# Kernel tuning notes

Measured on AMD Instinct MI355X. Metric: run time of the kernel, lower is better.

## Reference

```python
import jax, jax.numpy as jnp
import numpy as np

K = 3
PAD = 1
KK = K * K
GROUPS = 32  # min(32, dim) with dim=64
EPS = 1e-5


def _conv(x, w, pad):
    return jax.lax.conv_general_dilated(
        x, w, (1, 1), [(pad, pad), (pad, pad)],
        dimension_numbers=('NCHW', 'OIHW', 'NCHW'))


def _bilinear_gather(x, py, px):
    # x: (B,C,H,W); py,px: (B,KK,H,W) float sampling coords (zero pad outside)
    B, C, H, W = x.shape
    xf = x.reshape(B, C, H * W)
    y0f = jnp.floor(py)
    x0f = jnp.floor(px)
    wy1 = py - y0f  # fractional weights (differentiable path to offsets)
    wx1 = px - x0f
    y0 = y0f.astype(jnp.int32)
    x0 = x0f.astype(jnp.int32)

    def g(yi, xi):
        valid = (yi >= 0) & (yi < H) & (xi >= 0) & (xi < W)
        idx = (jnp.clip(yi, 0, H - 1) * W + jnp.clip(xi, 0, W - 1)).reshape(B, 1, -1)
        v = jnp.take_along_axis(xf, idx, axis=2).reshape(B, C, KK, H, W)
        return v * valid[:, None].astype(x.dtype)

    v00 = g(y0, x0)
    v01 = g(y0, x0 + 1)
    v10 = g(y0 + 1, x0)
    v11 = g(y0 + 1, x0 + 1)
    wy1e = wy1[:, None]
    wx1e = wx1[:, None]
    return (v00 * (1 - wy1e) * (1 - wx1e) + v01 * (1 - wy1e) * wx1e
            + v10 * wy1e * (1 - wx1e) + v11 * wy1e * wx1e)


def _forward(x, w_off1, w_off2, w_mask1, w_mask2, weight, bias, gamma, beta):
    B, C, H, W = x.shape
    # offset branch: 1x1 conv then KxK conv -> (B, 2*KK, H, W)
    off = _conv(_conv(x, w_off1, 0), w_off2, PAD).reshape(B, KK, 2, H, W)
    # mask branch -> sigmoid modulation (B, KK, H, W)
    mask = jax.nn.sigmoid(_conv(_conv(x, w_mask1, 0), w_mask2, PAD))
    # base kernel grid (torchvision deform_conv2d: pairs are (dy, dx) per tap)
    ky = jnp.repeat(jnp.arange(K) - PAD, K).astype(x.dtype)
    kx = jnp.tile(jnp.arange(K) - PAD, K).astype(x.dtype)
    py = off[:, :, 0] + jnp.arange(H, dtype=x.dtype)[None, None, :, None] + ky[None, :, None, None]
    px = off[:, :, 1] + jnp.arange(W, dtype=x.dtype)[None, None, None, :] + kx[None, :, None, None]
    samp = _bilinear_gather(x, py, px)  # (B, C, KK, H, W)
    # depthwise deformable conv: per-channel weight over KK taps, modulated by mask
    out = jnp.einsum('bkhw,ck,bckhw->bchw', mask, weight.reshape(C, KK), samp)
    out = out + bias[None, :, None, None]
    # GroupNorm(32, C)
    g = out.reshape(B, GROUPS, C // GROUPS, H, W)
    mu = g.mean(axis=(2, 3, 4), keepdims=True)
    var = g.var(axis=(2, 3, 4), keepdims=True)
    gn = ((g - mu) * jax.lax.rsqrt(var + EPS)).reshape(B, C, H, W)
    gn = gn * gamma[None, :, None, None] + beta[None, :, None, None]
    return jax.nn.gelu(gn, approximate=False)


def setup_inputs() -> dict:
    key = jax.random.key(0)
    ks = jax.random.split(key, 6)
    B, C, H, W = 4, 64, 128, 128
    x = jax.random.normal(ks[0], (B, C, H, W), dtype=jnp.float32)
    w_off1 = jax.random.normal(ks[1], (C, C, 1, 1), dtype=jnp.float32) * 0.05
    w_off2 = jax.random.normal(ks[2], (2 * KK, C, K, K), dtype=jnp.float32) * 0.02
    w_mask1 = jax.random.normal(ks[3], (C, C, 1, 1), dtype=jnp.float32) * 0.05
    w_mask2 = jax.random.normal(ks[4], (KK, C, K, K), dtype=jnp.float32) * 0.05
    bound = 1.0 / np.sqrt(KK)  # kaiming_uniform(a=1) for (C,1,K,K) -> fan_in=KK
    weight = jax.random.uniform(ks[5], (C, 1, K, K), dtype=jnp.float32,
                                minval=-bound, maxval=bound)
    bias = jnp.zeros((C,), dtype=jnp.float32)
    gamma = jnp.ones((C,), dtype=jnp.float32)
    beta = jnp.zeros((C,), dtype=jnp.float32)
    return {'x': x, 'w_off1': w_off1, 'w_off2': w_off2, 'w_mask1': w_mask1,
            'w_mask2': w_mask2, 'weight': weight, 'bias': bias,
            'gamma': gamma, 'beta': beta}


def reference(x, w_off1, w_off2, w_mask1, w_mask2, weight, bias, gamma, beta):
    return _forward(x, w_off1, w_off2, w_mask1, w_mask2, weight, bias, gamma, beta)
```

## Files before the change

### kernel.cpp

```cpp
#include <hip/hip_runtime.h>
#include <math.h>

#define B_  4
#define C_  64
#define H_  128
#define W_  128
#define HW_ (H_*W_)
#define NPIX_ (B_*HW_)
#define GROUPS_ 32

typedef __attribute__((ext_vector_type(8))) short short8;
typedef __attribute__((ext_vector_type(4))) float f32x4;

__device__ inline short f2bf_rne(float f) {
    unsigned u = __float_as_uint(f);
    unsigned r = (u + 0x7FFFu + ((u >> 16) & 1u)) >> 16;
    return (short)r;
}
__device__ inline float bf2f(short h) {
    return __uint_as_float(((unsigned)(unsigned short)h) << 16);
}
__device__ inline short8 ld8(const short* p) {
    union { uint4 u; short8 s; } c;
    c.u = *(const uint4*)p;
    return c.s;
}

__global__ void k0_prep(const float* __restrict__ w_off1, const float* __restrict__ w_mask1,
                        const float* __restrict__ w_off2, const float* __restrict__ w_mask2,
                        short* __restrict__ wc_hi, short* __restrict__ wc_lo) {
    int i = blockIdx.x * 256 + threadIdx.x;
    if (i >= 32 * 576) return;
    int cout = i / 576;
    int r    = i % 576;
    int pos  = r >> 6, ci = r & 63;
    float s = 0.f;
    if (cout < 18) {
        for (int cm = 0; cm < 64; cm++)
            s += w_off2[(cout * 64 + cm) * 9 + pos] * w_off1[cm * 64 + ci];
    } else if (cout < 27) {
        for (int cm = 0; cm < 64; cm++)
            s += w_mask2[((cout - 18) * 64 + cm) * 9 + pos] * w_mask1[cm * 64 + ci];
    }
    short h = f2bf_rne(s);
    wc_hi[i] = h;
    wc_lo[i] = f2bf_rne(s - bf2f(h));
}

__global__ __launch_bounds__(256) void k1_trans(const float* __restrict__ x,
                                                short* __restrict__ xtb) {
    int l   = threadIdx.x & 63;
    int wv  = threadIdx.x >> 6;
    int row = l >> 4, col = l & 15;
    int p0  = blockIdx.x * 64 + wv * 16;
    int b   = p0 >> 14;
    int hw  = p0 & (HW_ - 1);
    const float* xb = x + (size_t)b * C_ * HW_ + hw;
#pragma unroll
    for (int kb = 0; kb < 2; kb++) {
        int ci0 = kb * 32 + row * 8;
        float xv[8];
#pragma unroll
        for (int j = 0; j < 8; j++) xv[j] = xb[(ci0 + j) * HW_ + col];
        short8 a;
#pragma unroll
        for (int j = 0; j < 8; j++) a[j] = f2bf_rne(xv[j]);
        union { short8 s; uint4 u; } cv; cv.s = a;
        *(uint4*)(xtb + ((size_t)(p0 + col)) * 64 + ci0) = cv.u;
    }
}

__global__ __launch_bounds__(256, 2) void k2_mfma(const short* __restrict__ xtb,
                                                  const short* __restrict__ wc_hi,
                                                  const short* __restrict__ wc_lo,
                                                  float* __restrict__ offmask) {
    int l   = threadIdx.x & 63;
    int wv  = threadIdx.x >> 6;
    int row = l >> 4, col = l & 15;
    int blk = blockIdx.x;
    int h   = blk & 127;
    int pb  = blk * 128 + wv * 32;
    int w0  = (pb & 127);

    const short8 zero = {0,0,0,0,0,0,0,0};
    f32x4 a00 = {0.f,0.f,0.f,0.f};
    f32x4 a01 = {0.f,0.f,0.f,0.f};
    f32x4 a10 = {0.f,0.f,0.f,0.f};
    f32x4 a11 = {0.f,0.f,0.f,0.f};

    short8 cw0, cw1, cw2, cw3, ca0, ca1;
    {
        const int pos = 0, dy = -1, dx = -1;
        int ci0 = row * 8;
        int ko  = pos * 64 + ci0;
        cw0 = ld8(wc_hi + (size_t)col * 576 + ko);
        cw1 = ld8(wc_lo + (size_t)col * 576 + ko);
        cw2 = ld8(wc_hi + (size_t)(col + 16) * 576 + ko);
        cw3 = ld8(wc_lo + (size_t)(col + 16) * 576 + ko);
#pragma unroll
        for (int mt = 0; mt < 2; mt++) {
            int pbase = pb + mt * 16 + col;
            int w = w0 + mt * 16 + col;
            bool valid = ((unsigned)(h + dy) < 128u) && ((unsigned)(w + dx) < 128u);
            int addr = valid ? (pbase + dy * 128 + dx) : pbase;
            short8 v = ld8(xtb + (size_t)addr * 64 + ci0);
            if (mt == 0) ca0 = valid ? v : zero; else ca1 = valid ? v : zero;
        }
    }

#pragma unroll
    for (int kb = 0; kb < 18; kb++) {
        short8 nw0, nw1, nw2, nw3, na0, na1;
        if (kb < 17) {
            const int kn = kb + 1;
            const int pos = kn >> 1;
            const int dy = pos / 3 - 1, dx = pos % 3 - 1;
            int ci0 = (kn & 1) * 32 + row * 8;
            int ko  = pos * 64 + ci0;
            nw0 = ld8(wc_hi + (size_t)col * 576 + ko);
            nw1 = ld8(wc_lo + (size_t)col * 576 + ko);
            nw2 = ld8(wc_hi + (size_t)(col + 16) * 576 + ko);
            nw3 = ld8(wc_lo + (size_t)(col + 16) * 576 + ko);
#pragma unroll
            for (int mt = 0; mt < 2; mt++) {
                int pbase = pb + mt * 16 + col;
                int w = w0 + mt * 16 + col;
                bool valid = ((unsigned)(h + dy) < 128u) && ((unsigned)(w + dx) < 128u);
                int addr = valid ? (pbase + dy * 128 + dx) : pbase;
                short8 v = ld8(xtb + (size_t)addr * 64 + ci0);
                if (mt == 0) na0 = valid ? v : zero; else na1 = valid ? v : zero;
            }
        }
        a00 = __builtin_amdgcn_mfma_f32_16x16x32_bf16(ca0, cw0, a00, 0, 0, 0);
        a00 = __builtin_amdgcn_mfma_f32_16x16x32_bf16(ca0, cw1, a00, 0, 0, 0);
        a01 = __builtin_amdgcn_mfma_f32_16x16x32_bf16(ca0, cw2, a01, 0, 0, 0);
        a01 = __builtin_amdgcn_mfma_f32_16x16x32_bf16(ca0, cw3, a01, 0, 0, 0);
        a10 = __builtin_amdgcn_mfma_f32_16x16x32_bf16(ca1, cw0, a10, 0, 0, 0);
        a10 = __builtin_amdgcn_mfma_f32_16x16x32_bf16(ca1, cw1, a10, 0, 0, 0);
        a11 = __builtin_amdgcn_mfma_f32_16x16x32_bf16(ca1, cw2, a11, 0, 0, 0);
        a11 = __builtin_amdgcn_mfma_f32_16x16x32_bf16(ca1, cw3, a11, 0, 0, 0);
        cw0 = nw0; cw1 = nw1; cw2 = nw2; cw3 = nw3;
        ca0 = na0; ca1 = na1;
    }

#pragma unroll
    for (int mt = 0; mt < 2; mt++) {
        f32x4 n0 = mt ? a10 : a00;
        f32x4 n1 = mt ? a11 : a01;
#pragma unroll
        for (int r = 0; r < 4; r++) {
            int p = pb + mt * 16 + row * 4 + r;
            float* om = offmask + (size_t)p * 32;
            om[col] = n0[r];
            if (col < 2)       om[16 + col] = n1[r];
            else if (col < 11) om[16 + col] = 1.f / (1.f + expf(-n1[r]));
        }
    }
}

__global__ __launch_bounds__(256) void k3_deform(const short* __restrict__ xtb,
                                                 const float* __restrict__ offmask,
                                                 const float* __restrict__ weight,
                                                 const float* __restrict__ bias,
                                                 unsigned short* __restrict__ out_pre,
                                                 float* __restrict__ partials) {
    __shared__ float wl[C_ * 9];
    __shared__ float bl[C_];
    __shared__ float lds_s[4][4][8];
    __shared__ float lds_ss[4][4][8];
    for (int i = threadIdx.x; i < C_ * 9; i += 256) wl[i] = weight[i];
    if (threadIdx.x < C_) bl[threadIdx.x] = bias[threadIdx.x];
    __syncthreads();

    int blk   = blockIdx.x;
    int xcd   = blk & 7;
    int slot  = blk >> 3;
    int b     = slot >> 5;
    int r     = (slot & 31) >> 1;
    int hrow  = slot & 1;
    int h     = xcd * 16 + r;
    int pl    = threadIdx.x >> 2;
    int chunk = threadIdx.x & 3;
    int c0    = chunk * 16;
    int w     = hrow * 64 + pl;
    int hw    = h * W_ + w;
    int P     = b * HW_ + hw;
    int slot_img = xcd * 32 + (slot & 31);

    float acc[16];
#pragma unroll
    for (int i = 0; i < 16; i++) acc[i] = 0.f;

    const float* po = offmask + (size_t)P * 32;
    const short* xb = xtb + (size_t)b * HW_ * 64;

    for (int k = 0; k < 9; k++) {
        float offy = po[2 * k];
        float offx = po[2 * k + 1];
        float mk   = po[18 + k];
        float py = offy + (float)h + (float)(k / 3 - 1);
        float px = offx + (float)w + (float)(k % 3 - 1);
        float y0f = floorf(py), x0f = floorf(px);
        int y0 = (int)y0f, x0 = (int)x0f;
        int y1 = y0 + 1,   x1 = x0 + 1;
        float wy1 = py - y0f, wx1 = px - x0f;
        float wy0 = 1.f - wy1, wx0 = 1.f - wx1;
        bool vy0 = ((unsigned)y0 < (unsigned)H_);
        bool vy1 = ((unsigned)y1 < (unsigned)H_);
        bool vx0 = ((unsigned)x0 < (unsigned)W_);
        bool vx1 = ((unsigned)x1 < (unsigned)W_);
        int cy0 = min(max(y0, 0), H_ - 1);
        int cy1 = min(max(y1, 0), H_ - 1);
        int cx0 = min(max(x0, 0), W_ - 1);
        int cx1 = min(max(x1, 0), W_ - 1);
        float b00 = wy0 * wx0 * ((vy0 && vx0) ? mk : 0.f);
        float b01 = wy0 * wx1 * ((vy0 && vx1) ? mk : 0.f);
        float b10 = wy1 * wx0 * ((vy1 && vx0) ? mk : 0.f);
        float b11 = wy1 * wx1 * ((vy1 && vx1) ? mk : 0.f);

        const short* p00 = xb + ((size_t)cy0 * W_ + cx0) * 64 + c0;
        const short* p01 = xb + ((size_t)cy0 * W_ + cx1) * 64 + c0;
        const short* p10 = xb + ((size_t)cy1 * W_ + cx0) * 64 + c0;
        const short* p11 = xb + ((size_t)cy1 * W_ + cx1) * 64 + c0;

#pragma unroll
        for (int half = 0; half < 2; half++) {
            uint4 u00 = *(const uint4*)(p00 + 8 * half);
            uint4 u01 = *(const uint4*)(p01 + 8 * half);
            uint4 u10 = *(const uint4*)(p10 + 8 * half);
            uint4 u11 = *(const uint4*)(p11 + 8 * half);
            unsigned a00[4] = {u00.x, u00.y, u00.z, u00.w};
            unsigned a01[4] = {u01.x, u01.y, u01.z, u01.w};
            unsigned a10[4] = {u10.x, u10.y, u10.z, u10.w};
            unsigned a11[4] = {u11.x, u11.y, u11.z, u11.w};
#pragma unroll
            for (int d = 0; d < 4; d++) {
                float s_lo = b00 * __uint_as_float(a00[d] << 16)
                           + b01 * __uint_as_float(a01[d] << 16)
                           + b10 * __uint_as_float(a10[d] << 16)
                           + b11 * __uint_as_float(a11[d] << 16);
                float s_hi = b00 * __uint_as_float(a00[d] & 0xFFFF0000u)
                           + b01 * __uint_as_float(a01[d] & 0xFFFF0000u)
                           + b10 * __uint_as_float(a10[d] & 0xFFFF0000u)
                           + b11 * __uint_as_float(a11[d] & 0xFFFF0000u);
                int c = 8 * half + 2 * d;
                acc[c]     += wl[(c0 + c) * 9 + k] * s_lo;
                acc[c + 1] += wl[(c0 + c + 1) * 9 + k] * s_hi;
            }
        }
    }

    unsigned short* op = out_pre + ((size_t)b * C_ + c0) * HW_ + hw;
#pragma unroll
    for (int c = 0; c < 16; c++) {
        acc[c] += bl[c0 + c];
        op[c * HW_] = (unsigned short)f2bf_rne(acc[c]);
    }

    float s8[8], ss8[8];
#pragma unroll
    for (int j = 0; j < 8; j++) {
        float a0 = acc[2 * j], a1 = acc[2 * j + 1];
        s8[j]  = a0 + a1;
        ss8[j] = a0 * a0 + a1 * a1;
    }
#pragma unroll
    for (int m = 4; m < 64; m <<= 1) {
#pragma unroll
        for (int j = 0; j < 8; j++) {
            s8[j]  += __shfl_xor(s8[j], m);
            ss8[j] += __shfl_xor(ss8[j], m);
        }
    }
    int lane = threadIdx.x & 63, wid = threadIdx.x >> 6;
    if (lane < 4) {
#pragma unroll
        for (int j = 0; j < 8; j++) {
            lds_s[wid][lane][j]  = s8[j];
            lds_ss[wid][lane][j] = ss8[j];
        }
    }
    __syncthreads();
    if (threadIdx.x < 32) {
        int g = threadIdx.x;
        int ch = g >> 3, j = g & 7;
        float S  = lds_s[0][ch][j] + lds_s[1][ch][j] + lds_s[2][ch][j] + lds_s[3][ch][j];
        float SS = lds_ss[0][ch][j] + lds_ss[1][ch][j] + lds_ss[2][ch][j] + lds_ss[3][ch][j];
        float2 v = make_float2(S, SS);
        *(float2*)(partials + (((size_t)(b * GROUPS_ + g)) * 256 + slot_img) * 2) = v;
    }
}

__global__ __launch_bounds__(256) void k4_reduce(const float* __restrict__ partials,
                                                 float* __restrict__ stats) {
    int bg = blockIdx.x;
    float2 v = ((const float2*)partials)[bg * 256 + threadIdx.x];
    float s = v.x, ss = v.y;
#pragma unroll
    for (int m = 1; m < 64; m <<= 1) {
        s  += __shfl_xor(s, m);
        ss += __shfl_xor(ss, m);
    }
    __shared__ float ls[8];
    int lane = threadIdx.x & 63, wid = threadIdx.x >> 6;
    if (lane == 0) { ls[wid] = s; ls[4 + wid] = ss; }
    __syncthreads();
    if (threadIdx.x == 0) {
        float S  = ls[0] + ls[1] + ls[2] + ls[3];
        float SS = ls[4] + ls[5] + ls[6] + ls[7];
        const float inv = 1.f / (2.f * HW_);
        float mean = S * inv;
        float var  = SS * inv - mean * mean;
        stats[bg * 2]     = mean;
        stats[bg * 2 + 1] = rsqrtf(var + 1e-5f);
    }
}

__global__ __launch_bounds__(256) void k5_norm_gelu(const unsigned short* __restrict__ out_pre,
                                                    const float* __restrict__ stats,
                                                    const float* __restrict__ gamma,
                                                    const float* __restrict__ beta,
                                                    float* __restrict__ out) {
    int i = blockIdx.x * 256 + threadIdx.x;
    int e = i << 3;
    int c = (e >> 14) & (C_ - 1);
    int b = e >> 20;
    int bg = b * GROUPS_ + (c >> 1);
    float mean = stats[bg * 2];
    float rstd = stats[bg * 2 + 1];
    float ga = gamma[c] * rstd;
    float be = beta[c] - mean * ga;
    uint4 v = ((const uint4*)out_pre)[i];
    unsigned dw[4] = {v.x, v.y, v.z, v.w};
    float4 r0, r1;
    float o[8];
#pragma unroll
    for (int d = 0; d < 4; d++) {
        float lo = __uint_as_float(dw[d] << 16);
        float hi = __uint_as_float(dw[d] & 0xFFFF0000u);
        float t0 = lo * ga + be;
        float t1 = hi * ga + be;
        o[2 * d]     = 0.5f * t0 * (1.f + erff(t0 * 0.70710678118654752f));
        o[2 * d + 1] = 0.5f * t1 * (1.f + erff(t1 * 0.70710678118654752f));
    }
    r0 = make_float4(o[0], o[1], o[2], o[3]);
    r1 = make_float4(o[4], o[5], o[6], o[7]);
    ((float4*)out)[2 * i]     = r0;
    ((float4*)out)[2 * i + 1] = r1;
}

extern "C" void kernel_launch(void* const* d_in, const int* in_sizes, int n_in,
                              void* d_out, int out_size, void* d_ws, size_t ws_size,
                              hipStream_t stream) {
    const float* x       = (const float*)d_in[0];
    const float* w_off1  = (const float*)d_in[1];
    const float* w_off2  = (const float*)d_in[2];
    const float* w_mask1 = (const float*)d_in[3];
    const float* w_mask2 = (const float*)d_in[4];
    const float* weight  = (const float*)d_in[5];
    const float* bias    = (const float*)d_in[6];
    const float* gamma   = (const float*)d_in[7];
    const float* beta    = (const float*)d_in[8];
    float* out = (float*)d_out;

    char* ws = (char*)d_ws;
    size_t o = 0;
    short* wc_hi = (short*)(ws + o); o += 32 * 576 * 2;
    short* wc_lo = (short*)(ws + o); o += 32 * 576 * 2;
    o = (o + 255) & ~(size_t)255;
    short* xtb               = (short*)(ws + o);          o += (size_t)NPIX_ * 64 * 2;
    float* offmask           = (float*)(ws + o);          o += (size_t)NPIX_ * 32 * 4;
    unsigned short* out_pre  = (unsigned short*)(ws + o); o += (size_t)NPIX_ * 64 * 2;
    float* partials          = (float*)(ws + o);          o += (size_t)128 * 256 * 2 * 4;
    float* stats             = (float*)(ws + o);          o += 256 * 4;

    hipLaunchKernelGGL(k0_prep, dim3(72), dim3(256), 0, stream,
                       w_off1, w_mask1, w_off2, w_mask2, wc_hi, wc_lo);
    hipLaunchKernelGGL(k1_trans, dim3(NPIX_ / 64), dim3(256), 0, stream,
                       x, xtb);
    hipLaunchKernelGGL(k2_mfma, dim3(NPIX_ / 128), dim3(256), 0, stream,
                       xtb, wc_hi, wc_lo, offmask);
    hipLaunchKernelGGL(k3_deform, dim3(NPIX_ / 64), dim3(256), 0, stream,
                       xtb, offmask, weight, bias, out_pre, partials);
    hipLaunchKernelGGL(k4_reduce, dim3(B_ * GROUPS_), dim3(256), 0, stream,
                       partials, stats);
    hipLaunchKernelGGL(k5_norm_gelu, dim3(NPIX_ * 64 / 8 / 256), dim3(256), 0, stream,
                       out_pre, stats, gamma, beta, out);
}
```

Before: 146.0 us.

## Drop split-bf16 weight residual, fuse weight prep into transpose, preload weights

```diff
diff --git a/kernel.cpp b/kernel.cpp
--- a/kernel.cpp
+++ b/kernel.cpp
@@ -17,38 +17,37 @@
     unsigned r = (u + 0x7FFFu + ((u >> 16) & 1u)) >> 16;
     return (short)r;
 }
-__device__ inline float bf2f(short h) {
-    return __uint_as_float(((unsigned)(unsigned short)h) << 16);
-}
 __device__ inline short8 ld8(const short* p) {
     union { uint4 u; short8 s; } c;
     c.u = *(const uint4*)p;
     return c.s;
 }
 
-__global__ void k0_prep(const float* __restrict__ w_off1, const float* __restrict__ w_mask1,
-                        const float* __restrict__ w_off2, const float* __restrict__ w_mask2,
-                        short* __restrict__ wc_hi, short* __restrict__ wc_lo) {
-    int i = blockIdx.x * 256 + threadIdx.x;
-    if (i >= 32 * 576) return;
-    int cout = i / 576;
-    int r    = i % 576;
-    int pos  = r >> 6, ci = r & 63;
-    float s = 0.f;
-    if (cout < 18) {
-        for (int cm = 0; cm < 64; cm++)
-            s += w_off2[(cout * 64 + cm) * 9 + pos] * w_off1[cm * 64 + ci];
-    } else if (cout < 27) {
-        for (int cm = 0; cm < 64; cm++)
-            s += w_mask2[((cout - 18) * 64 + cm) * 9 + pos] * w_mask1[cm * 64 + ci];
-    }
-    short h = f2bf_rne(s);
-    wc_hi[i] = h;
-    wc_lo[i] = f2bf_rne(s - bf2f(h));
-}
-
-__global__ __launch_bounds__(256) void k1_trans(const float* __restrict__ x,
-                                                short* __restrict__ xtb) {
+__global__ __launch_bounds__(256) void k01(const float* __restrict__ x,
+                                           const float* __restrict__ w_off1,
+                                           const float* __restrict__ w_mask1,
+                                           const float* __restrict__ w_off2,
+                                           const float* __restrict__ w_mask2,
+                                           short* __restrict__ xtb,
+                                           short* __restrict__ wc_hi) {
+    if (blockIdx.x >= 1024) {
+        int i = (blockIdx.x - 1024) * 256 + threadIdx.x;
+        if (i < 32 * 576) {
+            int cout = i / 576;
+            int r    = i % 576;
+            int pos  = r >> 6, ci = r & 63;
+            float s = 0.f;
+            if (cout < 18) {
+                for (int cm = 0; cm < 64; cm++)
+                    s += w_off2[(cout * 64 + cm) * 9 + pos] * w_off1[cm * 64 + ci];
+            } else if (cout < 27) {
+                for (int cm = 0; cm < 64; cm++)
+                    s += w_mask2[((cout - 18) * 64 + cm) * 9 + pos] * w_mask1[cm * 64 + ci];
+            }
+            wc_hi[i] = f2bf_rne(s);
+        }
+        return;
+    }
     int l   = threadIdx.x & 63;
     int wv  = threadIdx.x >> 6;
     int row = l >> 4, col = l & 15;
@@ -72,7 +71,6 @@
 
 __global__ __launch_bounds__(256, 2) void k2_mfma(const short* __restrict__ xtb,
                                                   const short* __restrict__ wc_hi,
-                                                  const short* __restrict__ wc_lo,
                                                   float* __restrict__ offmask) {
     int l   = threadIdx.x & 63;
     int wv  = threadIdx.x >> 6;
@@ -82,21 +80,26 @@
     int pb  = blk * 128 + wv * 32;
     int w0  = (pb & 127);
 
+    short8 wfr[18][2];
+#pragma unroll
+    for (int kb = 0; kb < 18; kb++) {
+        int pos = kb >> 1;
+        int ci0 = (kb & 1) * 32 + row * 8;
+        int ko  = pos * 64 + ci0;
+        wfr[kb][0] = ld8(wc_hi + (size_t)col * 576 + ko);
+        wfr[kb][1] = ld8(wc_hi + (size_t)(col + 16) * 576 + ko);
+    }
+
     const short8 zero = {0,0,0,0,0,0,0,0};
     f32x4 a00 = {0.f,0.f,0.f,0.f};
     f32x4 a01 = {0.f,0.f,0.f,0.f};
     f32x4 a10 = {0.f,0.f,0.f,0.f};
     f32x4 a11 = {0.f,0.f,0.f,0.f};
 
-    short8 cw0, cw1, cw2, cw3, ca0, ca1;
+    short8 ca0, ca1;
     {
-        const int pos = 0, dy = -1, dx = -1;
+        const int dy = -1, dx = -1;
         int ci0 = row * 8;
-        int ko  = pos * 64 + ci0;
-        cw0 = ld8(wc_hi + (size_t)col * 576 + ko);
-        cw1 = ld8(wc_lo + (size_t)col * 576 + ko);
-        cw2 = ld8(wc_hi + (size_t)(col + 16) * 576 + ko);
-        cw3 = ld8(wc_lo + (size_t)(col + 16) * 576 + ko);
 #pragma unroll
         for (int mt = 0; mt < 2; mt++) {
             int pbase = pb + mt * 16 + col;
@@ -110,17 +113,12 @@
 
 #pragma unroll
     for (int kb = 0; kb < 18; kb++) {
-        short8 nw0, nw1, nw2, nw3, na0, na1;
+        short8 na0, na1;
         if (kb < 17) {
             const int kn = kb + 1;
             const int pos = kn >> 1;
             const int dy = pos / 3 - 1, dx = pos % 3 - 1;
             int ci0 = (kn & 1) * 32 + row * 8;
-            int ko  = pos * 64 + ci0;
-            nw0 = ld8(wc_hi + (size_t)col * 576 + ko);
-            nw1 = ld8(wc_lo + (size_t)col * 576 + ko);
-            nw2 = ld8(wc_hi + (size_t)(col + 16) * 576 + ko);
-            nw3 = ld8(wc_lo + (size_t)(col + 16) * 576 + ko);
 #pragma unroll
             for (int mt = 0; mt < 2; mt++) {
                 int pbase = pb + mt * 16 + col;
@@ -131,15 +129,10 @@
                 if (mt == 0) na0 = valid ? v : zero; else na1 = valid ? v : zero;
             }
         }
-        a00 = __builtin_amdgcn_mfma_f32_16x16x32_bf16(ca0, cw0, a00, 0, 0, 0);
-        a00 = __builtin_amdgcn_mfma_f32_16x16x32_bf16(ca0, cw1, a00, 0, 0, 0);
-        a01 = __builtin_amdgcn_mfma_f32_16x16x32_bf16(ca0, cw2, a01, 0, 0, 0);
-        a01 = __builtin_amdgcn_mfma_f32_16x16x32_bf16(ca0, cw3, a01, 0, 0, 0);
-        a10 = __builtin_amdgcn_mfma_f32_16x16x32_bf16(ca1, cw0, a10, 0, 0, 0);
-        a10 = __builtin_amdgcn_mfma_f32_16x16x32_bf16(ca1, cw1, a10, 0, 0, 0);
-        a11 = __builtin_amdgcn_mfma_f32_16x16x32_bf16(ca1, cw2, a11, 0, 0, 0);
-        a11 = __builtin_amdgcn_mfma_f32_16x16x32_bf16(ca1, cw3, a11, 0, 0, 0);
-        cw0 = nw0; cw1 = nw1; cw2 = nw2; cw3 = nw3;
+        a00 = __builtin_amdgcn_mfma_f32_16x16x32_bf16(ca0, wfr[kb][0], a00, 0, 0, 0);
+        a01 = __builtin_amdgcn_mfma_f32_16x16x32_bf16(ca0, wfr[kb][1], a01, 0, 0, 0);
+        a10 = __builtin_amdgcn_mfma_f32_16x16x32_bf16(ca1, wfr[kb][0], a10, 0, 0, 0);
+        a11 = __builtin_amdgcn_mfma_f32_16x16x32_bf16(ca1, wfr[kb][1], a11, 0, 0, 0);
         ca0 = na0; ca1 = na1;
     }
 
@@ -332,7 +325,6 @@
     float be = beta[c] - mean * ga;
     uint4 v = ((const uint4*)out_pre)[i];
     unsigned dw[4] = {v.x, v.y, v.z, v.w};
-    float4 r0, r1;
     float o[8];
 #pragma unroll
     for (int d = 0; d < 4; d++) {
@@ -343,10 +335,8 @@
         o[2 * d]     = 0.5f * t0 * (1.f + erff(t0 * 0.70710678118654752f));
         o[2 * d + 1] = 0.5f * t1 * (1.f + erff(t1 * 0.70710678118654752f));
     }
-    r0 = make_float4(o[0], o[1], o[2], o[3]);
-    r1 = make_float4(o[4], o[5], o[6], o[7]);
-    ((float4*)out)[2 * i]     = r0;
-    ((float4*)out)[2 * i + 1] = r1;
+    ((float4*)out)[2 * i]     = make_float4(o[0], o[1], o[2], o[3]);
+    ((float4*)out)[2 * i + 1] = make_float4(o[4], o[5], o[6], o[7]);
 }
 
 extern "C" void kernel_launch(void* const* d_in, const int* in_sizes, int n_in,
@@ -366,7 +356,6 @@
     char* ws = (char*)d_ws;
     size_t o = 0;
     short* wc_hi = (short*)(ws + o); o += 32 * 576 * 2;
-    short* wc_lo = (short*)(ws + o); o += 32 * 576 * 2;
     o = (o + 255) & ~(size_t)255;
     short* xtb               = (short*)(ws + o);          o += (size_t)NPIX_ * 64 * 2;
     float* offmask           = (float*)(ws + o);          o += (size_t)NPIX_ * 32 * 4;
@@ -374,12 +363,10 @@
     float* partials          = (float*)(ws + o);          o += (size_t)128 * 256 * 2 * 4;
     float* stats             = (float*)(ws + o);          o += 256 * 4;
 
-    hipLaunchKernelGGL(k0_prep, dim3(72), dim3(256), 0, stream,
-                       w_off1, w_mask1, w_off2, w_mask2, wc_hi, wc_lo);
-    hipLaunchKernelGGL(k1_trans, dim3(NPIX_ / 64), dim3(256), 0, stream,
-                       x, xtb);
+    hipLaunchKernelGGL(k01, dim3(1024 + 72), dim3(256), 0, stream,
+                       x, w_off1, w_mask1, w_off2, w_mask2, xtb, wc_hi);
     hipLaunchKernelGGL(k2_mfma, dim3(NPIX_ / 128), dim3(256), 0, stream,
-                       xtb, wc_hi, wc_lo, offmask);
+                       xtb, wc_hi, offmask);
     hipLaunchKernelGGL(k3_deform, dim3(NPIX_ / 64), dim3(256), 0, stream,
                        xtb, offmask, weight, bias, out_pre, partials);
     hipLaunchKernelGGL(k4_reduce, dim3(B_ * GROUPS_), dim3(256), 0, stream,
```

Measured after the change: 136.0 us. -6.9%, faster.
